# Kernel tuning notes

Measured on AMD Instinct MI355X. Metric: run time of the kernel, lower is better.

The kernel has to match this reference:

```python
import jax, jax.numpy as jnp
import numpy as np

B, S, I, H, O, L = 64, 1024, 256, 512, 512, 2


def setup_inputs() -> dict:
    key = jax.random.key(0)
    ks = jax.random.split(key, 12)
    s_in = 1.0 / np.sqrt(H)
    inp = {
        "x": jax.random.normal(ks[0], (B, S, I), dtype=jnp.float32),
        "W_ih0": jax.random.uniform(ks[1], (3 * H, I), jnp.float32, -s_in, s_in),
        "W_hh0": jax.random.uniform(ks[2], (3 * H, H), jnp.float32, -s_in, s_in),
        "b_ih0": jax.random.uniform(ks[3], (3 * H,), jnp.float32, -s_in, s_in),
        "b_hh0": jax.random.uniform(ks[4], (3 * H,), jnp.float32, -s_in, s_in),
        "W_ih1": jax.random.uniform(ks[5], (3 * H, H), jnp.float32, -s_in, s_in),
        "W_hh1": jax.random.uniform(ks[6], (3 * H, H), jnp.float32, -s_in, s_in),
        "b_ih1": jax.random.uniform(ks[7], (3 * H,), jnp.float32, -s_in, s_in),
        "b_hh1": jax.random.uniform(ks[8], (3 * H,), jnp.float32, -s_in, s_in),
        "W_fc": jax.random.uniform(ks[9], (O, H), jnp.float32, -s_in, s_in),
        "b_fc": jax.random.uniform(ks[10], (O,), jnp.float32, -s_in, s_in),
    }
    return inp


def _gru_cell(x_t, h, W_ih, W_hh, b_ih, b_hh):
    # standard torch GRUCell: gates order (r, z, n)
    gi = x_t @ W_ih.T + b_ih  # [B, 3H]
    gh = h @ W_hh.T + b_hh    # [B, 3H]
    i_r, i_z, i_n = jnp.split(gi, 3, axis=-1)
    h_r, h_z, h_n = jnp.split(gh, 3, axis=-1)
    r = jax.nn.sigmoid(i_r + h_r)
    z = jax.nn.sigmoid(i_z + h_z)
    n = jnp.tanh(i_n + r * h_n)
    return (1.0 - z) * n + z * h


def reference(x, W_ih0, W_hh0, b_ih0, b_hh0, W_ih1, W_hh1, b_ih1, b_hh1, W_fc, b_fc):
    b = x.shape[0]
    h0 = jnp.zeros((b, H), dtype=x.dtype)
    h1 = jnp.zeros((b, H), dtype=x.dtype)

    def step(carry, x_t):
        h0, h1 = carry
        h0n = _gru_cell(x_t, h0, W_ih0, W_hh0, b_ih0, b_hh0)
        h1n = _gru_cell(h0n, h1, W_ih1, W_hh1, b_ih1, b_hh1)
        return (h0n, h1n), h1n

    (h0f, h1f), ys = jax.lax.scan(step, (h0, h1), jnp.swapaxes(x, 0, 1))
    out = jnp.swapaxes(ys, 0, 1)  # [B, S, H]
    logits = out @ W_fc.T + b_fc  # [B, S, O]
    hidden = jnp.stack([h0f, h1f])  # [L, B, H]
    return logits, hidden
```

## Files before the change

### kernel.cpp

```cpp
#include <hip/hip_runtime.h>


typedef unsigned short u16;
typedef unsigned long long u64;
typedef __attribute__((ext_vector_type(8))) short bf16x8;
typedef __attribute__((ext_vector_type(4))) float f32x4;

#define B_ 64
#define S_ 1024
#define I_ 256
#define H_ 512
#define O_ 512
#define NBLK 64

#define MFMA_(a, b, c) __builtin_amdgcn_mfma_f32_16x16x32_bf16((a), (b), (c), 0, 0, 0)

__device__ __forceinline__ u16 f2bf(float f) {
  union { float f; unsigned u; } v; v.f = f;
  unsigned r = v.u + 0x7fffu + ((v.u >> 16) & 1u);
  return (u16)(r >> 16);
}

__device__ __forceinline__ float sigmoidf_(float x) {
  return 1.0f / (1.0f + __expf(-x));
}

__device__ __forceinline__ void store_sc1_u64(void* p, u64 v) {
  __hip_atomic_store((u64*)p, v, __ATOMIC_RELAXED, __HIP_MEMORY_SCOPE_AGENT);
}

__device__ __forceinline__ void grid_bar(unsigned* slots, unsigned target) {
  __syncthreads();
  if (threadIdx.x < 64) {
    if (threadIdx.x == 0) {
      __hip_atomic_store(slots + ((unsigned)blockIdx.x << 4), target,
                         __ATOMIC_RELAXED, __HIP_MEMORY_SCOPE_AGENT);
    }
    const unsigned* myslot = slots + ((unsigned)threadIdx.x << 4);
    unsigned v;
    do {
      v = __hip_atomic_load(myslot, __ATOMIC_RELAXED, __HIP_MEMORY_SCOPE_AGENT);
      if (v < target) __builtin_amdgcn_s_sleep(2);
    } while (v < target);
    if (threadIdx.x == 0)
      __builtin_amdgcn_fence(__ATOMIC_ACQUIRE, "agent");
  }
  __syncthreads();
}

template<int NK, int LAYER>
__device__ void layer_run(
    const u16* __restrict__ xin,
    const float* __restrict__ Wih, const float* __restrict__ Whh,
    const float* __restrict__ bih, const float* __restrict__ bhh,
    u16* __restrict__ hself,
    u16* __restrict__ ybf,
    float* __restrict__ outh,
    float (*dump)[4][4][256], float* hst, float (*bias_s)[16], unsigned* slots)
{
  const int tid = threadIdx.x;
  const int wave = tid >> 6, lane = tid & 63, lm = lane & 15, quad = lane >> 4;
  const int U0 = (blockIdx.x & 31) << 4;
  const int Kx = (LAYER == 0) ? I_ : H_;
  const int KW = NK * 32;
  const int wbase = wave * KW;

  if (tid < 16) {
    bias_s[0][tid] = bih[U0 + tid] + bhh[U0 + tid];
    bias_s[1][tid] = bih[H_ + U0 + tid] + bhh[H_ + U0 + tid];
    bias_s[2][tid] = bih[2 * H_ + U0 + tid];
    bias_s[3][tid] = bhh[2 * H_ + U0 + tid];
  }
  #pragma unroll
  for (int j = 0; j < 4; ++j) hst[tid + j * 256] = 0.f;

  bf16x8 Bfr[3][NK];
  int aoffb[NK], astr16[NK];
  bool insel[NK], isx[NK];
  #pragma unroll
  for (int ks = 0; ks < NK; ++ks) {
    const int kb = wbase + ks * 32;
    const bool xr = (kb < Kx);
    insel[ks] = xr; isx[ks] = xr;
    const int col = (xr ? kb : kb - Kx) + quad * 8;
    const int stride = xr ? ((LAYER == 0) ? I_ : H_) : H_;
    aoffb[ks] = lm * stride + col;
    astr16[ks] = stride << 4;
    #pragma unroll
    for (int g = 0; g < 3; ++g) {
      const int row = g * H_ + U0 + lm;
      const float* src = xr ? (Wih + (size_t)row * Kx + kb + quad * 8)
                            : (Whh + (size_t)row * H_ + (kb - Kx) + quad * 8);
      float4 lo = *(const float4*)src;
      float4 hi = *(const float4*)(src + 4);
      bf16x8 v;
      v[0] = (short)f2bf(lo.x); v[1] = (short)f2bf(lo.y);
      v[2] = (short)f2bf(lo.z); v[3] = (short)f2bf(lo.w);
      v[4] = (short)f2bf(hi.x); v[5] = (short)f2bf(hi.y);
      v[6] = (short)f2bf(hi.z); v[7] = (short)f2bf(hi.w);
      Bfr[g][ks] = v;
    }
  }
  __syncthreads();

  for (unsigned i = 0; i <= S_; ++i) {
    const bool active = (LAYER == 0) ? (i < S_) : (i >= 1);
    if (active) {
      const int t = (LAYER == 0) ? (int)i : (int)i - 1;
      const u16* ain = (LAYER == 0) ? (xin + (size_t)t * (B_ * I_))
                                    : (xin + (size_t)(t & 1) * (B_ * H_));
      const u16* aself = hself + (size_t)((t - 1) & 1) * (B_ * H_);

      bf16x8 Afr[NK][4];
      #pragma unroll
      for (int ks = 0; ks < NK; ++ks) {
        const u16* p = (insel[ks] ? ain : aself) + aoffb[ks];
        Afr[ks][0] = *(const bf16x8*)(p);
        Afr[ks][1] = *(const bf16x8*)(p + astr16[ks]);
        Afr[ks][2] = *(const bf16x8*)(p + 2 * astr16[ks]);
        Afr[ks][3] = *(const bf16x8*)(p + 3 * astr16[ks]);
      }

      f32x4 aR[4] = {}, aZ[4] = {}, aNx[4] = {}, aNh[4] = {};
      #pragma unroll
      for (int ks = 0; ks < NK; ++ks) {
        aR[0] = MFMA_(Afr[ks][0], Bfr[0][ks], aR[0]);
        aR[1] = MFMA_(Afr[ks][1], Bfr[0][ks], aR[1]);
        aR[2] = MFMA_(Afr[ks][2], Bfr[0][ks], aR[2]);
        aR[3] = MFMA_(Afr[ks][3], Bfr[0][ks], aR[3]);
        aZ[0] = MFMA_(Afr[ks][0], Bfr[1][ks], aZ[0]);
        aZ[1] = MFMA_(Afr[ks][1], Bfr[1][ks], aZ[1]);
        aZ[2] = MFMA_(Afr[ks][2], Bfr[1][ks], aZ[2]);
        aZ[3] = MFMA_(Afr[ks][3], Bfr[1][ks], aZ[3]);
        if (isx[ks]) {
          aNx[0] = MFMA_(Afr[ks][0], Bfr[2][ks], aNx[0]);
          aNx[1] = MFMA_(Afr[ks][1], Bfr[2][ks], aNx[1]);
          aNx[2] = MFMA_(Afr[ks][2], Bfr[2][ks], aNx[2]);
          aNx[3] = MFMA_(Afr[ks][3], Bfr[2][ks], aNx[3]);
        } else {
          aNh[0] = MFMA_(Afr[ks][0], Bfr[2][ks], aNh[0]);
          aNh[1] = MFMA_(Afr[ks][1], Bfr[2][ks], aNh[1]);
          aNh[2] = MFMA_(Afr[ks][2], Bfr[2][ks], aNh[2]);
          aNh[3] = MFMA_(Afr[ks][3], Bfr[2][ks], aNh[3]);
        }
      }

      #pragma unroll
      for (int mt = 0; mt < 4; ++mt) {
        *(f32x4*)&dump[wave][0][mt][lane << 2] = aR[mt];
        *(f32x4*)&dump[wave][1][mt][lane << 2] = aZ[mt];
        *(f32x4*)&dump[wave][2][mt][lane << 2] = aNx[mt];
        *(f32x4*)&dump[wave][3][mt][lane << 2] = aNh[mt];
      }
      __syncthreads();

      u16* hpub = hself + (size_t)(t & 1) * (B_ * H_);
      {
        const int m = tid >> 2, u4 = (tid & 3) << 2;
        const int mt = m >> 4;
        u16 hb4[4];
        float hf4[4];
        #pragma unroll
        for (int j = 0; j < 4; ++j) {
          const int u = u4 + j;
          const int idx = ((m & 12) << 4) | (u << 2) | (m & 3);
          float r = 0.f, z = 0.f, nx = 0.f, nh = 0.f;
          #pragma unroll
          for (int w = 0; w < 4; ++w) {
            r  += dump[w][0][mt][idx];
            z  += dump[w][1][mt][idx];
            nx += dump[w][2][mt][idx];
            nh += dump[w][3][mt][idx];
          }
          r = sigmoidf_(r + bias_s[0][u]);
          z = sigmoidf_(z + bias_s[1][u]);
          const float nn = tanhf(nx + bias_s[2][u] + r * (nh + bias_s[3][u]));
          const float hp = hst[(m << 4) | u];
          const float hn = (1.f - z) * nn + z * hp;
          hst[(m << 4) | u] = hn;
          hb4[j] = f2bf(hn);
          hf4[j] = hn;
        }
        const u64 pk = (u64)hb4[0] | ((u64)hb4[1] << 16) |
                       ((u64)hb4[2] << 32) | ((u64)hb4[3] << 48);
        store_sc1_u64(hpub + m * H_ + U0 + u4, pk);
        if (LAYER == 1)
          store_sc1_u64(ybf + ((size_t)m * S_ + t) * H_ + U0 + u4, pk);
        if (t == S_ - 1) {
          union { float f[2]; u64 u; } o0, o1;
          o0.f[0] = hf4[0]; o0.f[1] = hf4[1];
          o1.f[0] = hf4[2]; o1.f[1] = hf4[3];
          store_sc1_u64(outh + m * H_ + U0 + u4, o0.u);
          store_sc1_u64(outh + m * H_ + U0 + u4 + 2, o1.u);
        }
      }
    }
    grid_bar(slots, i + 1);
  }
}

__global__ __launch_bounds__(256, 1) void gru_persistent(
    const u16* __restrict__ x_bf,
    const float* __restrict__ Wih0, const float* __restrict__ Whh0,
    const float* __restrict__ bih0, const float* __restrict__ bhh0,
    const float* __restrict__ Wih1, const float* __restrict__ Whh1,
    const float* __restrict__ bih1, const float* __restrict__ bhh1,
    u16* __restrict__ h0buf, u16* __restrict__ h1buf,
    u16* __restrict__ ybf, float* __restrict__ outh, unsigned* slots)
{
  __shared__ float dump[4][4][4][256];
  __shared__ float hst[1024];
  __shared__ float bias_s[4][16];
  if (blockIdx.x < 32)
    layer_run<6, 0>(x_bf, Wih0, Whh0, bih0, bhh0, h0buf, (u16*)nullptr,
                    outh, dump, hst, bias_s, slots);
  else
    layer_run<8, 1>(h0buf, Wih1, Whh1, bih1, bhh1, h1buf, ybf,
                    outh + B_ * H_, dump, hst, bias_s, slots);
}

__global__ void conv_x(const float* __restrict__ src, u16* __restrict__ dst) {
  const int idx = blockIdx.x * 256 + threadIdx.x;
  const int c4 = idx & 63, tt = (idx >> 6) & 1023, b = idx >> 16;
  float4 v = *(const float4*)(src + (((size_t)(b << 10) | tt) << 8) + (c4 << 2));
  ushort4 o;
  o.x = f2bf(v.x); o.y = f2bf(v.y); o.z = f2bf(v.z); o.w = f2bf(v.w);
  *(ushort4*)(dst + (((size_t)(tt << 6) | b) << 8) + (c4 << 2)) = o;
}

__global__ void conv_bf16(const float* __restrict__ src, u16* __restrict__ dst, int n4) {
  int i = blockIdx.x * blockDim.x + threadIdx.x;
  int stride = gridDim.x * blockDim.x;
  for (; i < n4; i += stride) {
    float4 v = ((const float4*)src)[i];
    ushort4 o;
    o.x = f2bf(v.x); o.y = f2bf(v.y); o.z = f2bf(v.z); o.w = f2bf(v.w);
    ((ushort4*)dst)[i] = o;
  }
}

__global__ __launch_bounds__(256) void fc_gemm(
    const u16* __restrict__ A, const u16* __restrict__ Bm,
    const float* __restrict__ bias, float* __restrict__ C)
{
  const int bid = blockIdx.x;
  const int bm = bid >> 2, bn = bid & 3;
  const int wave = threadIdx.x >> 6, lane = threadIdx.x & 63;
  const int wm = wave >> 1, wn = wave & 1;
  const int M0 = bm * 128 + wm * 64;
  const int N0 = bn * 128 + wn * 64;
  const int lm = lane & 15, quad = lane >> 4;

  f32x4 acc[4][4];
  #pragma unroll
  for (int j = 0; j < 4; ++j) {
    float bv = bias[N0 + j * 16 + lm];
    #pragma unroll
    for (int i = 0; i < 4; ++i) acc[i][j] = (f32x4){bv, bv, bv, bv};
  }

  const u16* a0 = A + (size_t)(M0 + lm) * 512 + quad * 8;
  const u16* b0 = Bm + (size_t)(N0 + lm) * 512 + quad * 8;
  for (int ks = 0; ks < 512; ks += 32) {
    bf16x8 af[4], bfr[4];
    #pragma unroll
    for (int i = 0; i < 4; ++i) af[i]  = *(const bf16x8*)(a0 + (size_t)i * 16 * 512 + ks);
    #pragma unroll
    for (int j = 0; j < 4; ++j) bfr[j] = *(const bf16x8*)(b0 + (size_t)j * 16 * 512 + ks);
    #pragma unroll
    for (int i = 0; i < 4; ++i)
      #pragma unroll
      for (int j = 0; j < 4; ++j)
        acc[i][j] = MFMA_(af[i], bfr[j], acc[i][j]);
  }

  #pragma unroll
  for (int i = 0; i < 4; ++i)
    #pragma unroll
    for (int j = 0; j < 4; ++j)
      #pragma unroll
      for (int r = 0; r < 4; ++r) {
        const int m = M0 + i * 16 + quad * 4 + r;
        const int n = N0 + j * 16 + lm;
        C[(size_t)m * 512 + n] = acc[i][j][r];
      }
}

extern "C" void kernel_launch(void* const* d_in, const int* in_sizes, int n_in,
                              void* d_out, int out_size, void* d_ws, size_t ws_size,
                              hipStream_t stream) {
  const float* x     = (const float*)d_in[0];
  const float* W_ih0 = (const float*)d_in[1];
  const float* W_hh0 = (const float*)d_in[2];
  const float* b_ih0 = (const float*)d_in[3];
  const float* b_hh0 = (const float*)d_in[4];
  const float* W_ih1 = (const float*)d_in[5];
  const float* W_hh1 = (const float*)d_in[6];
  const float* b_ih1 = (const float*)d_in[7];
  const float* b_hh1 = (const float*)d_in[8];
  const float* W_fc  = (const float*)d_in[9];
  const float* b_fc  = (const float*)d_in[10];
  float* out = (float*)d_out;

  char* ws = (char*)d_ws;
  const size_t OFF_XBF = 0;
  const size_t OFF_YBF = 33554432;
  const size_t OFF_WFC = 100663296;
  const size_t OFF_H0  = 101187584;
  const size_t OFF_H1  = 101318656;
  const size_t OFF_BAR = 101449728;

  u16* x_bf   = (u16*)(ws + OFF_XBF);
  u16* y_bf   = (u16*)(ws + OFF_YBF);
  u16* wfc_bf = (u16*)(ws + OFF_WFC);
  u16* h0buf  = (u16*)(ws + OFF_H0);
  u16* h1buf  = (u16*)(ws + OFF_H1);
  unsigned* slots = (unsigned*)(ws + OFF_BAR);

  hipMemsetAsync(ws + OFF_H0, 0, 131072 * 2 + 4096, stream);

  conv_x<<<16384, 256, 0, stream>>>(x, x_bf);
  conv_bf16<<<256, 256, 0, stream>>>(W_fc, wfc_bf, (O_ * H_) / 4);

  gru_persistent<<<NBLK, 256, 0, stream>>>(
      x_bf, W_ih0, W_hh0, b_ih0, b_hh0, W_ih1, W_hh1, b_ih1, b_hh1,
      h0buf, h1buf, y_bf, out + (size_t)B_ * S_ * O_, slots);

  fc_gemm<<<2048, 256, 0, stream>>>(y_bf, wfc_bf, b_fc, out);
}
```

Before: 7.364 ms.

## Use 32-deep hidden-state ring to issue acquire fence only every 16 steps

Replaces the double-buffered hidden-state buffers with 32-slot ring buffers per layer. The agent-scope acquire fence (cache invalidate) in the grid barrier now runs only every 16th step instead of every step. Because a ring slot is rewritten only 32 steps after its last use, an invalidate always falls between a slot's reuse and its next read, so stale cached lines should not be observed. This removes most per-step cache invalidation on the critical serial path. In exchange it uses more workspace and a larger memset, and correctness now rests on this ring-period argument and on relaxed loads not being reordered.

```diff
diff --git a/kernel.cpp b/kernel.cpp
--- a/kernel.cpp
+++ b/kernel.cpp
@@ -12,6 +12,8 @@
 #define H_ 512
 #define O_ 512
 #define NBLK 64
+#define RING 32
+#define INVP 16
 
 #define MFMA_(a, b, c) __builtin_amdgcn_mfma_f32_16x16x32_bf16((a), (b), (c), 0, 0, 0)
 
@@ -29,7 +31,8 @@
   __hip_atomic_store((u64*)p, v, __ATOMIC_RELAXED, __HIP_MEMORY_SCOPE_AGENT);
 }
 
-__device__ __forceinline__ void grid_bar(unsigned* slots, unsigned target) {
+__device__ __forceinline__ void grid_bar(unsigned* slots, unsigned target,
+                                         bool doInv) {
   __syncthreads();
   if (threadIdx.x < 64) {
     if (threadIdx.x == 0) {
@@ -42,7 +45,7 @@
       v = __hip_atomic_load(myslot, __ATOMIC_RELAXED, __HIP_MEMORY_SCOPE_AGENT);
       if (v < target) __builtin_amdgcn_s_sleep(2);
     } while (v < target);
-    if (threadIdx.x == 0)
+    if (doInv && threadIdx.x == 0)
       __builtin_amdgcn_fence(__ATOMIC_ACQUIRE, "agent");
   }
   __syncthreads();
@@ -53,7 +56,7 @@
     const u16* __restrict__ xin,
     const float* __restrict__ Wih, const float* __restrict__ Whh,
     const float* __restrict__ bih, const float* __restrict__ bhh,
-    u16* __restrict__ hself,
+    u16* __restrict__ hring,
     u16* __restrict__ ybf,
     float* __restrict__ outh,
     float (*dump)[4][4][256], float* hst, float (*bias_s)[16], unsigned* slots)
@@ -107,9 +110,10 @@
     const bool active = (LAYER == 0) ? (i < S_) : (i >= 1);
     if (active) {
       const int t = (LAYER == 0) ? (int)i : (int)i - 1;
-      const u16* ain = (LAYER == 0) ? (xin + (size_t)t * (B_ * I_))
-                                    : (xin + (size_t)(t & 1) * (B_ * H_));
-      const u16* aself = hself + (size_t)((t - 1) & 1) * (B_ * H_);
+      const u16* ain = (LAYER == 0)
+          ? (xin + (size_t)t * (B_ * I_))
+          : (xin + (size_t)(t & (RING - 1)) * (B_ * H_));
+      const u16* aself = hring + (size_t)((t - 1) & (RING - 1)) * (B_ * H_);
 
       bf16x8 Afr[NK][4];
       #pragma unroll
@@ -154,7 +158,7 @@
       }
       __syncthreads();
 
-      u16* hpub = hself + (size_t)(t & 1) * (B_ * H_);
+      u16* hpub = hring + (size_t)(t & (RING - 1)) * (B_ * H_);
       {
         const int m = tid >> 2, u4 = (tid & 3) << 2;
         const int mt = m >> 4;
@@ -195,7 +199,7 @@
         }
       }
     }
-    grid_bar(slots, i + 1);
+    grid_bar(slots, i + 1, (i & (INVP - 1)) == (INVP - 1));
   }
 }
 
@@ -205,17 +209,17 @@
     const float* __restrict__ bih0, const float* __restrict__ bhh0,
     const float* __restrict__ Wih1, const float* __restrict__ Whh1,
     const float* __restrict__ bih1, const float* __restrict__ bhh1,
-    u16* __restrict__ h0buf, u16* __restrict__ h1buf,
+    u16* __restrict__ h0ring, u16* __restrict__ h1ring,
     u16* __restrict__ ybf, float* __restrict__ outh, unsigned* slots)
 {
   __shared__ float dump[4][4][4][256];
   __shared__ float hst[1024];
   __shared__ float bias_s[4][16];
   if (blockIdx.x < 32)
-    layer_run<6, 0>(x_bf, Wih0, Whh0, bih0, bhh0, h0buf, (u16*)nullptr,
+    layer_run<6, 0>(x_bf, Wih0, Whh0, bih0, bhh0, h0ring, (u16*)nullptr,
                     outh, dump, hst, bias_s, slots);
   else
-    layer_run<8, 1>(h0buf, Wih1, Whh1, bih1, bhh1, h1buf, ybf,
+    layer_run<8, 1>(h0ring, Wih1, Whh1, bih1, bhh1, h1ring, ybf,
                     outh + B_ * H_, dump, hst, bias_s, slots);
 }
 
@@ -307,24 +311,24 @@
   const size_t OFF_YBF = 33554432;
   const size_t OFF_WFC = 100663296;
   const size_t OFF_H0  = 101187584;
-  const size_t OFF_H1  = 101318656;
-  const size_t OFF_BAR = 101449728;
+  const size_t OFF_H1  = 103284736;
+  const size_t OFF_BAR = 105381888;
 
   u16* x_bf   = (u16*)(ws + OFF_XBF);
   u16* y_bf   = (u16*)(ws + OFF_YBF);
   u16* wfc_bf = (u16*)(ws + OFF_WFC);
-  u16* h0buf  = (u16*)(ws + OFF_H0);
-  u16* h1buf  = (u16*)(ws + OFF_H1);
+  u16* h0ring = (u16*)(ws + OFF_H0);
+  u16* h1ring = (u16*)(ws + OFF_H1);
   unsigned* slots = (unsigned*)(ws + OFF_BAR);
 
-  hipMemsetAsync(ws + OFF_H0, 0, 131072 * 2 + 4096, stream);
+  hipMemsetAsync(ws + OFF_H0, 0, 2097152 * 2 + 4096, stream);
 
   conv_x<<<16384, 256, 0, stream>>>(x, x_bf);
   conv_bf16<<<256, 256, 0, stream>>>(W_fc, wfc_bf, (O_ * H_) / 4);
 
   gru_persistent<<<NBLK, 256, 0, stream>>>(
       x_bf, W_ih0, W_hh0, b_ih0, b_hh0, W_ih1, W_hh1, b_ih1, b_hh1,
-      h0buf, h1buf, y_bf, out + (size_t)B_ * S_ * O_, slots);
+      h0ring, h1ring, y_bf, out + (size_t)B_ * S_ * O_, slots);
 
   fc_gemm<<<2048, 256, 0, stream>>>(y_bf, wfc_bf, b_fc, out);
 }
```

New measurement: 7.058 ms. 1.04x faster.
